# Kernel optimization log

Hardware: AMD Instinct MI355X
Metric: run time of the kernel (lower is better)

The kernel has to match this reference:

```python
import jax, jax.numpy as jnp
import numpy as np

ALPHA = 1.0

def setup_inputs() -> dict:
    key = jax.random.key(0)
    k1, k2 = jax.random.split(key)
    B, T, F = 8, 4096, 1024
    x = jax.random.normal(k1, (B, T, F), dtype=jnp.float32)
    # ragged valid lengths in [T//2, T]; mask[b, t] = t < length[b]
    lengths = jax.random.randint(k2, (B,), T // 2, T + 1)
    attention_mask = (jnp.arange(T)[None, :] < lengths[:, None]).astype(jnp.int32)
    return {"input_values": x, "attention_mask": attention_mask}


def reference(input_values, attention_mask):
    # input_values: [B,T,F]; attention_mask: [B,T] (1 for valid, 0 for pad)
    m = attention_mask.astype(input_values.dtype)[..., None]          # [B,T,1]
    L = jnp.sum(m, axis=1)                                            # [B,1]
    # k: per-channel mean over valid timesteps (torch mean over dims [-1,-2])
    k = jnp.sum(input_values * m, axis=1) / L                         # [B,F]
    k_centered = k - jnp.mean(k, axis=-1, keepdims=True)              # [B,F] (center over channels)
    kd = jnp.sqrt(jnp.sum(k_centered ** 2, axis=-1, keepdims=True))   # [B,1]
    # center each timestep over channels
    x_centered = input_values - jnp.mean(input_values, axis=-1, keepdims=True)  # [B,T,F]
    qd = jnp.sqrt(jnp.sum(x_centered ** 2, axis=-1))                  # [B,T]
    num = jnp.einsum('btf,bf->bt', x_centered, k_centered)            # [B,T]
    C_qk = num / (qd * kd)                                            # [B,T]
    A = (1.0 - jax.nn.sigmoid(C_qk)) ** ALPHA                         # [B,T]
    # apply attention and zero out padded positions (original zero-pads)
    out = input_values * A[..., None] * m                             # [B,T,F]
    return out
```

## Files before the change

### kernel.cpp

```cpp
#include <hip/hip_runtime.h>
#include <math.h>

#define BB 8
#define TT 4096
#define FF 1024
#define F4 (FF / 4)
#define TS 128
#define TCHUNK (TT / TS)

typedef float vfloat4 __attribute__((ext_vector_type(4)));

__global__ __launch_bounds__(256) void k1_partial(const float4* __restrict__ x4,
                                                  const int* __restrict__ mask,
                                                  float4* __restrict__ part4) {
    int ts  = blockIdx.x;
    int b   = blockIdx.y;
    int tid = threadIdx.x;

    __shared__ float msh[TCHUNK];
    if (tid < TCHUNK) msh[tid] = (float)mask[(size_t)b * TT + (size_t)ts * TCHUNK + tid];
    __syncthreads();

    const float4* xb = x4 + ((size_t)b * TT + (size_t)ts * TCHUNK) * F4 + tid;
    float4 acc = make_float4(0.f, 0.f, 0.f, 0.f);
    #pragma unroll 8
    for (int t = 0; t < TCHUNK; ++t) {
        float4 v = xb[(size_t)t * F4];
        float  m = msh[t];
        acc.x = fmaf(m, v.x, acc.x);
        acc.y = fmaf(m, v.y, acc.y);
        acc.z = fmaf(m, v.z, acc.z);
        acc.w = fmaf(m, v.w, acc.w);
    }
    part4[((size_t)b * TS + ts) * F4 + tid] = acc;
}

__global__ __launch_bounds__(1024) void k2_stats(const float* __restrict__ part,
                                                 const int* __restrict__ mask,
                                                 float* __restrict__ kc,
                                                 float* __restrict__ kd_arr,
                                                 float* __restrict__ skc_arr) {
    __shared__ float redA[16];
    __shared__ float redB[16];
    __shared__ float Lsh, meansh;

    int b    = blockIdx.x;
    int tid  = threadIdx.x;
    int wave = tid >> 6;
    int lane = tid & 63;

    int cnt = 0;
    #pragma unroll
    for (int i = 0; i < 4; ++i) cnt += mask[(size_t)b * TT + tid + i * 1024];
    float fc = (float)cnt;
    #pragma unroll
    for (int off = 32; off; off >>= 1) fc += __shfl_xor(fc, off);
    if (lane == 0) redA[wave] = fc;
    __syncthreads();
    if (tid == 0) {
        float s = 0.f;
        for (int i = 0; i < 16; ++i) s += redA[i];
        Lsh = s;
    }
    __syncthreads();
    float L = Lsh;

    float s = 0.f;
    #pragma unroll 8
    for (int ts = 0; ts < TS; ++ts) s += part[((size_t)b * TS + ts) * FF + tid];
    float k = s / L;

    float m = k;
    #pragma unroll
    for (int off = 32; off; off >>= 1) m += __shfl_xor(m, off);
    __syncthreads();
    if (lane == 0) redA[wave] = m;
    __syncthreads();
    if (tid == 0) {
        float t = 0.f;
        for (int i = 0; i < 16; ++i) t += redA[i];
        meansh = t * (1.0f / FF);
    }
    __syncthreads();
    float kcv = k - meansh;
    kc[(size_t)b * FF + tid] = kcv;

    float a  = kcv * kcv;
    float c2 = kcv;
    #pragma unroll
    for (int off = 32; off; off >>= 1) {
        a  += __shfl_xor(a, off);
        c2 += __shfl_xor(c2, off);
    }
    __syncthreads();
    if (lane == 0) { redA[wave] = a; redB[wave] = c2; }
    __syncthreads();
    if (tid == 0) {
        float sa = 0.f, sc = 0.f;
        for (int i = 0; i < 16; ++i) { sa += redA[i]; sc += redB[i]; }
        kd_arr[b]  = sqrtf(sa);
        skc_arr[b] = sc;
    }
}

__global__ __launch_bounds__(256) void k3_apply(const float4* __restrict__ x4,
                                                const int* __restrict__ mask,
                                                const float4* __restrict__ kc4,
                                                const float* __restrict__ kd_arr,
                                                const float* __restrict__ skc_arr,
                                                float4* __restrict__ out4) {
    int wave = threadIdx.x >> 6;
    int lane = threadIdx.x & 63;
    int t    = blockIdx.x * 4 + wave;
    int b    = blockIdx.y;
    size_t row = ((size_t)b * TT + t) * F4;

    vfloat4* orow = (vfloat4*)(out4 + row);
    if (mask[(size_t)b * TT + t] == 0) {
        vfloat4 z = (vfloat4)(0.f);
        #pragma unroll
        for (int j = 0; j < 4; ++j)
            __builtin_nontemporal_store(z, orow + lane + 64 * j);
        return;
    }

    const float4* xrow = x4 + row;
    const float4* krow = kc4 + (size_t)b * F4;
    float4 xv[4], kv[4];
    #pragma unroll
    for (int j = 0; j < 4; ++j) {
        xv[j] = xrow[lane + 64 * j];
        kv[j] = krow[lane + 64 * j];
    }

    float s1 = 0.f, s2 = 0.f, s3 = 0.f;
    #pragma unroll
    for (int j = 0; j < 4; ++j) {
        s1 += xv[j].x + xv[j].y + xv[j].z + xv[j].w;
        s2 = fmaf(xv[j].x, xv[j].x, fmaf(xv[j].y, xv[j].y,
             fmaf(xv[j].z, xv[j].z, fmaf(xv[j].w, xv[j].w, s2))));
        s3 = fmaf(xv[j].x, kv[j].x, fmaf(xv[j].y, kv[j].y,
             fmaf(xv[j].z, kv[j].z, fmaf(xv[j].w, kv[j].w, s3))));
    }
    #pragma unroll
    for (int off = 32; off; off >>= 1) {
        s1 += __shfl_xor(s1, off);
        s2 += __shfl_xor(s2, off);
        s3 += __shfl_xor(s3, off);
    }

    float mean = s1 * (1.0f / FF);
    float num  = s3 - mean * skc_arr[b];
    float qd2  = s2 - s1 * s1 * (1.0f / FF);
    float qd   = sqrtf(fmaxf(qd2, 0.f));
    float C    = num / (qd * kd_arr[b]);
    float A    = 1.0f / (1.0f + __expf(C));

    #pragma unroll
    for (int j = 0; j < 4; ++j) {
        vfloat4 o;
        o.x = xv[j].x * A; o.y = xv[j].y * A;
        o.z = xv[j].z * A; o.w = xv[j].w * A;
        __builtin_nontemporal_store(o, orow + lane + 64 * j);
    }
}

extern "C" void kernel_launch(void* const* d_in, const int* in_sizes, int n_in,
                              void* d_out, int out_size, void* d_ws, size_t ws_size,
                              hipStream_t stream) {
    const float* x    = (const float*)d_in[0];
    const int*   mask = (const int*)d_in[1];
    float*       out  = (float*)d_out;

    float* part = (float*)d_ws;
    float* kc   = part + (size_t)BB * TS * FF;
    float* kd   = kc + (size_t)BB * FF;
    float* skc  = kd + BB;

    k1_partial<<<dim3(TS, BB), 256, 0, stream>>>((const float4*)x, mask, (float4*)part);
    k2_stats<<<BB, 1024, 0, stream>>>(part, mask, kc, kd, skc);
    k3_apply<<<dim3(TT / 4, BB), 256, 0, stream>>>((const float4*)x, mask, (const float4*)kc,
                                                   kd, skc, (float4*)out);
}
```

Measured before the change: 255.0 us.

## Fuse three passes into one cooperative kernel with grid syncs

Replaces the partial-sum, stats and apply kernels with a single cooperative kernel of 1024 blocks that uses grid.sync between phases. Each block reads only the valid prefix of its chunk for the partial sums, the stats phase is spread over 256 blocks using atomics, and kd is computed from sum and sum-of-squares of k. The apply phase revisits the same chunk in reverse row order, hoping to reuse cached x. This removes launch overhead and the serial 8-block stats kernel, at the cost of grid-wide barriers and a reliance on all 1024 blocks being co-resident.

New measurement: 458.9 us. +79.9%, slower.

```diff
diff --git a/kernel.cpp b/kernel.cpp
--- a/kernel.cpp
+++ b/kernel.cpp
@@ -1,4 +1,5 @@
 #include <hip/hip_runtime.h>
+#include <hip/hip_cooperative_groups.h>
 #include <math.h>
 
 #define BB 8
@@ -7,178 +8,170 @@
 #define F4 (FF / 4)
 #define TS 128
 #define TCHUNK (TT / TS)
+#define NBLK (BB * TS)
+
+namespace cg = cooperative_groups;
 
 typedef float vfloat4 __attribute__((ext_vector_type(4)));
 
-__global__ __launch_bounds__(256) void k1_partial(const float4* __restrict__ x4,
-                                                  const int* __restrict__ mask,
-                                                  float4* __restrict__ part4) {
-    int ts  = blockIdx.x;
-    int b   = blockIdx.y;
-    int tid = threadIdx.x;
+__global__ __launch_bounds__(256, 4) void fused_all(
+    const float4* __restrict__ x4,
+    const int*    __restrict__ mask,
+    float4*       __restrict__ out4,
+    float*        __restrict__ part,
+    float*        __restrict__ kbuf,
+    float*        __restrict__ Sk,
+    float*        __restrict__ Skk)
+{
+    cg::grid_group grid = cg::this_grid();
+    const int tid  = threadIdx.x;
+    const int wave = tid >> 6;
+    const int lane = tid & 63;
+    const int blk  = blockIdx.x;
+    const int b    = blk & 7;
+    const int ts   = blk >> 3;
 
     __shared__ float msh[TCHUNK];
-    if (tid < TCHUNK) msh[tid] = (float)mask[(size_t)b * TT + (size_t)ts * TCHUNK + tid];
-    __syncthreads();
+    __shared__ float red[8][32];
 
-    const float4* xb = x4 + ((size_t)b * TT + (size_t)ts * TCHUNK) * F4 + tid;
-    float4 acc = make_float4(0.f, 0.f, 0.f, 0.f);
-    #pragma unroll 8
-    for (int t = 0; t < TCHUNK; ++t) {
-        float4 v = xb[(size_t)t * F4];
-        float  m = msh[t];
-        acc.x = fmaf(m, v.x, acc.x);
-        acc.y = fmaf(m, v.y, acc.y);
-        acc.z = fmaf(m, v.z, acc.z);
-        acc.w = fmaf(m, v.w, acc.w);
-    }
-    part4[((size_t)b * TS + ts) * F4 + tid] = acc;
-}
-
-__global__ __launch_bounds__(1024) void k2_stats(const float* __restrict__ part,
-                                                 const int* __restrict__ mask,
-                                                 float* __restrict__ kc,
-                                                 float* __restrict__ kd_arr,
-                                                 float* __restrict__ skc_arr) {
-    __shared__ float redA[16];
-    __shared__ float redB[16];
-    __shared__ float Lsh, meansh;
-
-    int b    = blockIdx.x;
-    int tid  = threadIdx.x;
-    int wave = tid >> 6;
-    int lane = tid & 63;
-
-    int cnt = 0;
-    #pragma unroll
-    for (int i = 0; i < 4; ++i) cnt += mask[(size_t)b * TT + tid + i * 1024];
-    float fc = (float)cnt;
-    #pragma unroll
-    for (int off = 32; off; off >>= 1) fc += __shfl_xor(fc, off);
-    if (lane == 0) redA[wave] = fc;
-    __syncthreads();
-    if (tid == 0) {
-        float s = 0.f;
-        for (int i = 0; i < 16; ++i) s += redA[i];
-        Lsh = s;
-    }
-    __syncthreads();
-    float L = Lsh;
-
-    float s = 0.f;
-    #pragma unroll 8
-    for (int ts = 0; ts < TS; ++ts) s += part[((size_t)b * TS + ts) * FF + tid];
-    float k = s / L;
-
-    float m = k;
-    #pragma unroll
-    for (int off = 32; off; off >>= 1) m += __shfl_xor(m, off);
-    __syncthreads();
-    if (lane == 0) redA[wave] = m;
-    __syncthreads();
-    if (tid == 0) {
-        float t = 0.f;
-        for (int i = 0; i < 16; ++i) t += redA[i];
-        meansh = t * (1.0f / FF);
-    }
-    __syncthreads();
-    float kcv = k - meansh;
-    kc[(size_t)b * FF + tid] = kcv;
-
-    float a  = kcv * kcv;
-    float c2 = kcv;
-    #pragma unroll
-    for (int off = 32; off; off >>= 1) {
-        a  += __shfl_xor(a, off);
-        c2 += __shfl_xor(c2, off);
-    }
-    __syncthreads();
-    if (lane == 0) { redA[wave] = a; redB[wave] = c2; }
-    __syncthreads();
-    if (tid == 0) {
-        float sa = 0.f, sc = 0.f;
-        for (int i = 0; i < 16; ++i) { sa += redA[i]; sc += redB[i]; }
-        kd_arr[b]  = sqrtf(sa);
-        skc_arr[b] = sc;
-    }
-}
-
-__global__ __launch_bounds__(256) void k3_apply(const float4* __restrict__ x4,
-                                                const int* __restrict__ mask,
-                                                const float4* __restrict__ kc4,
-                                                const float* __restrict__ kd_arr,
-                                                const float* __restrict__ skc_arr,
-                                                float4* __restrict__ out4) {
-    int wave = threadIdx.x >> 6;
-    int lane = threadIdx.x & 63;
-    int t    = blockIdx.x * 4 + wave;
-    int b    = blockIdx.y;
-    size_t row = ((size_t)b * TT + t) * F4;
-
-    vfloat4* orow = (vfloat4*)(out4 + row);
-    if (mask[(size_t)b * TT + t] == 0) {
-        vfloat4 z = (vfloat4)(0.f);
-        #pragma unroll
-        for (int j = 0; j < 4; ++j)
-            __builtin_nontemporal_store(z, orow + lane + 64 * j);
-        return;
+    if (blk == 0 && tid < 2 * BB) {
+        if (tid < BB) Sk[tid]       = 0.f;
+        else          Skk[tid - BB] = 0.f;
     }
 
-    const float4* xrow = x4 + row;
-    const float4* krow = kc4 + (size_t)b * F4;
-    float4 xv[4], kv[4];
+    if (tid < TCHUNK) msh[tid] = (float)mask[(size_t)b * TT + ts * TCHUNK + tid];
+    __syncthreads();
+    int nv = 0;
     #pragma unroll
-    for (int j = 0; j < 4; ++j) {
-        xv[j] = xrow[lane + 64 * j];
-        kv[j] = krow[lane + 64 * j];
+    for (int i = 0; i < TCHUNK; ++i) nv += (msh[i] != 0.f) ? 1 : 0;
+
+    if (nv > 0) {
+        const float4* xb = x4 + ((size_t)b * TT + (size_t)ts * TCHUNK) * F4 + tid;
+        float4 acc = make_float4(0.f, 0.f, 0.f, 0.f);
+        #pragma unroll 8
+        for (int t = 0; t < nv; ++t) {
+            float4 v = xb[(size_t)t * F4];
+            acc.x += v.x; acc.y += v.y; acc.z += v.z; acc.w += v.w;
+        }
+        ((float4*)part)[((size_t)b * TS + ts) * F4 + tid] = acc;
     }
 
-    float s1 = 0.f, s2 = 0.f, s3 = 0.f;
-    #pragma unroll
-    for (int j = 0; j < 4; ++j) {
-        s1 += xv[j].x + xv[j].y + xv[j].z + xv[j].w;
-        s2 = fmaf(xv[j].x, xv[j].x, fmaf(xv[j].y, xv[j].y,
-             fmaf(xv[j].z, xv[j].z, fmaf(xv[j].w, xv[j].w, s2))));
-        s3 = fmaf(xv[j].x, kv[j].x, fmaf(xv[j].y, kv[j].y,
-             fmaf(xv[j].z, kv[j].z, fmaf(xv[j].w, kv[j].w, s3))));
-    }
-    #pragma unroll
-    for (int off = 32; off; off >>= 1) {
-        s1 += __shfl_xor(s1, off);
-        s2 += __shfl_xor(s2, off);
-        s3 += __shfl_xor(s3, off);
+    grid.sync();
+
+    if (blk < 256) {
+        const int b2    = blk >> 5;
+        const int fbase = (blk & 31) * 32;
+
+        int c = 0;
+        #pragma unroll
+        for (int i = 0; i < 16; ++i) c += mask[(size_t)b2 * TT + tid + 256 * i];
+        float fc = (float)c;
+        #pragma unroll
+        for (int off = 32; off; off >>= 1) fc += __shfl_xor(fc, off);
+        if (lane == 0) red[0][wave] = fc;
+        __syncthreads();
+        const float Lf  = red[0][0] + red[0][1] + red[0][2] + red[0][3];
+        const int   nts = ((int)Lf + TCHUNK - 1) / TCHUNK;
+        __syncthreads();
+
+        const int f     = fbase + (tid & 31);
+        const int slice = tid >> 5;
+        float s = 0.f;
+        for (int t = slice; t < nts; t += 8)
+            s += part[((size_t)b2 * TS + t) * FF + f];
+        red[slice][tid & 31] = s;
+        __syncthreads();
+        if (tid < 32) {
+            float sum = 0.f;
+            #pragma unroll
+            for (int sl = 0; sl < 8; ++sl) sum += red[sl][tid];
+            const float kv = sum / Lf;
+            kbuf[(size_t)b2 * FF + fbase + tid] = kv;
+            float a = kv, q = kv * kv;
+            #pragma unroll
+            for (int off = 16; off; off >>= 1) {
+                a += __shfl_xor(a, off);
+                q += __shfl_xor(q, off);
+            }
+            if (tid == 0) {
+                atomicAdd(&Sk[b2],  a);
+                atomicAdd(&Skk[b2], q);
+            }
+        }
     }
 
-    float mean = s1 * (1.0f / FF);
-    float num  = s3 - mean * skc_arr[b];
-    float qd2  = s2 - s1 * s1 * (1.0f / FF);
-    float qd   = sqrtf(fmaxf(qd2, 0.f));
-    float C    = num / (qd * kd_arr[b]);
-    float A    = 1.0f / (1.0f + __expf(C));
+    grid.sync();
 
+    const float sk  = Sk[b];
+    const float skk = Skk[b];
+    const float kd  = sqrtf(fmaxf(skk - sk * sk * (1.0f / FF), 0.f));
+
+    const float4* kb4 = (const float4*)(kbuf + (size_t)b * FF);
+    float4 kv[4];
     #pragma unroll
-    for (int j = 0; j < 4; ++j) {
-        vfloat4 o;
-        o.x = xv[j].x * A; o.y = xv[j].y * A;
-        o.z = xv[j].z * A; o.w = xv[j].w * A;
-        __builtin_nontemporal_store(o, orow + lane + 64 * j);
+    for (int j = 0; j < 4; ++j) kv[j] = kb4[lane + 64 * j];
+
+    const size_t chunkbase = ((size_t)b * TT + (size_t)ts * TCHUNK) * F4;
+    for (int i = 7; i >= 0; --i) {
+        const int r = wave * 8 + i;
+        const size_t row = chunkbase + (size_t)r * F4;
+        vfloat4* orow = (vfloat4*)(out4 + row);
+        if (msh[r] == 0.f) {
+            vfloat4 z = (vfloat4)(0.f);
+            #pragma unroll
+            for (int j = 0; j < 4; ++j)
+                __builtin_nontemporal_store(z, orow + lane + 64 * j);
+            continue;
+        }
+        const float4* xrow = x4 + row;
+        float4 xv[4];
+        #pragma unroll
+        for (int j = 0; j < 4; ++j) xv[j] = xrow[lane + 64 * j];
+
+        float s1 = 0.f, s2 = 0.f, s3 = 0.f;
+        #pragma unroll
+        for (int j = 0; j < 4; ++j) {
+            s1 += xv[j].x + xv[j].y + xv[j].z + xv[j].w;
+            s2 = fmaf(xv[j].x, xv[j].x, fmaf(xv[j].y, xv[j].y,
+                 fmaf(xv[j].z, xv[j].z, fmaf(xv[j].w, xv[j].w, s2))));
+            s3 = fmaf(xv[j].x, kv[j].x, fmaf(xv[j].y, kv[j].y,
+                 fmaf(xv[j].z, kv[j].z, fmaf(xv[j].w, kv[j].w, s3))));
+        }
+        #pragma unroll
+        for (int off = 32; off; off >>= 1) {
+            s1 += __shfl_xor(s1, off);
+            s2 += __shfl_xor(s2, off);
+            s3 += __shfl_xor(s3, off);
+        }
+        const float mx  = s1 * (1.0f / FF);
+        const float num = s3 - mx * sk;
+        const float qd  = sqrtf(fmaxf(s2 - s1 * s1 * (1.0f / FF), 0.f));
+        const float C   = num / (qd * kd);
+        const float A   = 1.0f / (1.0f + __expf(C));
+        #pragma unroll
+        for (int j = 0; j < 4; ++j) {
+            vfloat4 o;
+            o.x = xv[j].x * A; o.y = xv[j].y * A;
+            o.z = xv[j].z * A; o.w = xv[j].w * A;
+            __builtin_nontemporal_store(o, orow + lane + 64 * j);
+        }
     }
 }
 
 extern "C" void kernel_launch(void* const* d_in, const int* in_sizes, int n_in,
                               void* d_out, int out_size, void* d_ws, size_t ws_size,
                               hipStream_t stream) {
-    const float* x    = (const float*)d_in[0];
-    const int*   mask = (const int*)d_in[1];
-    float*       out  = (float*)d_out;
+    const float4* x4   = (const float4*)d_in[0];
+    const int*    mask = (const int*)d_in[1];
+    float4*       out4 = (float4*)d_out;
 
     float* part = (float*)d_ws;
-    float* kc   = part + (size_t)BB * TS * FF;
-    float* kd   = kc + (size_t)BB * FF;
-    float* skc  = kd + BB;
+    float* kbuf = part + (size_t)BB * TS * FF;
+    float* Sk   = kbuf + (size_t)BB * FF;
+    float* Skk  = Sk + BB;
 
-    k1_partial<<<dim3(TS, BB), 256, 0, stream>>>((const float4*)x, mask, (float4*)part);
-    k2_stats<<<BB, 1024, 0, stream>>>(part, mask, kc, kd, skc);
-    k3_apply<<<dim3(TT / 4, BB), 256, 0, stream>>>((const float4*)x, mask, (const float4*)kc,
-                                                   kd, skc, (float4*)out);
+    void* args[] = { (void*)&x4, (void*)&mask, (void*)&out4,
+                     (void*)&part, (void*)&kbuf, (void*)&Sk, (void*)&Skk };
+    hipLaunchCooperativeKernel((const void*)fused_all, dim3(NBLK), dim3(256),
+                               args, 0, stream);
 }
```
